# Kernel tuning notes

Hardware: AMD Instinct MI355X
Metric: run time of the kernel (lower is better)

## Reference

```python
import jax, jax.numpy as jnp
import numpy as np

N = 50000          # nodes
E = 1_600_000      # edges (avg degree 32)
D = 128            # input_dim
H = 128            # hidden_dim
EPS = 1e-5


def setup_inputs() -> dict:
    key = jax.random.key(0)
    ks = jax.random.split(key, 8)
    x = jax.random.normal(ks[0], (N, D), jnp.float32)
    edge_index = jax.random.randint(ks[1], (2, E), 0, N)
    message = jax.random.normal(ks[2], (E, H), jnp.float32)

    def lin(k, fin, fout):
        return jax.random.normal(k, (fin, fout), jnp.float32) / np.sqrt(fin).astype(np.float32)

    return {
        "x": x,
        "message": message,
        "W1": lin(ks[3], D + 2 * H, H), "b1": jnp.zeros((H,), jnp.float32),
        "g1": jnp.ones((H,), jnp.float32), "be1": jnp.zeros((H,), jnp.float32),
        "W2": lin(ks[4], H, H), "b2": jnp.zeros((H,), jnp.float32),
        "g2": jnp.ones((H,), jnp.float32), "be2": jnp.zeros((H,), jnp.float32),
        "Wa": lin(ks[5], H, 1), "ba": jnp.zeros((1,), jnp.float32),
        "edge_index": edge_index,
    }


def _batchnorm(h, g, b):
    # training-mode BatchNorm1d: biased batch stats over the node dim
    mu = h.mean(axis=0)
    var = h.var(axis=0)
    return (h - mu) * jax.lax.rsqrt(var + EPS) * g + b


def reference(x, message, W1, b1, g1, be1, W2, b2, g2, be2, Wa, ba, edge_index):
    row, col = edge_index[0], edge_index[1]
    n = x.shape[0]

    def smax(idx):
        m = jax.ops.segment_max(message, idx, num_segments=n)  # [N, H]
        # torch_scatter scatter(reduce='max') leaves empty slots at 0
        return jnp.where(jnp.isfinite(m), m, jnp.zeros_like(m))

    fwd = smax(col)
    bwd = smax(row)
    out = jnp.concatenate([x, fwd, bwd], axis=1)  # [N, D+2H]

    h = jax.nn.relu(_batchnorm(out @ W1 + b1, g1, be1))  # dropout = identity (eval)
    h = jax.nn.relu(_batchnorm(h @ W2 + b2, g2, be2))
    att = jax.nn.sigmoid(h @ Wa + ba).reshape(-1)        # [N]
    return h, att
```

## Files before the change

### kernel.cpp

```cpp
#include <hip/hip_runtime.h>
#include <math.h>

#define N_NODES 50000
#define N_EDGES 1600000
#define DIM 128
#define EPS 1e-5f
#define CAP 96
#define CONVB 2048

typedef short bf16x8 __attribute__((ext_vector_type(8)));
typedef float f32x4 __attribute__((ext_vector_type(4)));
typedef int i32x4 __attribute__((ext_vector_type(4)));
typedef unsigned int u32x2 __attribute__((ext_vector_type(2)));
typedef unsigned short ushort_t;

__device__ __forceinline__ unsigned int f2bf(float f) {
    unsigned int u = __float_as_uint(f);
    return (u + 0x7FFFu + ((u >> 16) & 1u)) >> 16;
}
__device__ __forceinline__ float bf2f(ushort_t u) {
    return __uint_as_float(((unsigned int)u) << 16);
}

__device__ __forceinline__ void wmax(unsigned int w, float& lo, float& hi) {
    lo = fmaxf(lo, __uint_as_float(w << 16));
    hi = fmaxf(hi, __uint_as_float(w & 0xFFFF0000u));
}

__global__ __launch_bounds__(256) void k_prep(const float* __restrict__ W1, const float* __restrict__ W2,
                                              ushort_t* __restrict__ W1t, ushort_t* __restrict__ W2t) {
    int gid = blockIdx.x * 256 + threadIdx.x;
    if (gid < 128 * 384) {
        int j = gid / 384, k = gid % 384;
        W1t[gid] = (ushort_t)f2bf(W1[k * 128 + j]);
    } else {
        int g2 = gid - 128 * 384;
        if (g2 < 128 * 128) {
            int j = g2 / 128, k = g2 % 128;
            W2t[g2] = (ushort_t)f2bf(W2[k * 128 + j]);
        }
    }
}

__global__ __launch_bounds__(256) void k_bucketconv(const int* __restrict__ ei, int* __restrict__ cnt,
                                                    int* __restrict__ slots,
                                                    const f32x4* __restrict__ msg,
                                                    u32x2* __restrict__ msgb) {
    const int b = blockIdx.x;
    if (b & 1) {
        int t = (b >> 1) * 256 + threadIdx.x;
        if (t >= N_EDGES / 4) return;
        int4 r4 = reinterpret_cast<const int4*>(ei)[t];
        int4 c4 = reinterpret_cast<const int4*>(ei + N_EDGES)[t];
        int e = t * 4;
        slots[c4.x * CAP + atomicAdd(&cnt[c4.x], 1)] = e + 0;
        slots[c4.y * CAP + atomicAdd(&cnt[c4.y], 1)] = e + 1;
        slots[c4.z * CAP + atomicAdd(&cnt[c4.z], 1)] = e + 2;
        slots[c4.w * CAP + atomicAdd(&cnt[c4.w], 1)] = e + 3;
        slots[(N_NODES + r4.x) * CAP + atomicAdd(&cnt[N_NODES + r4.x], 1)] = e + 0;
        slots[(N_NODES + r4.y) * CAP + atomicAdd(&cnt[N_NODES + r4.y], 1)] = e + 1;
        slots[(N_NODES + r4.z) * CAP + atomicAdd(&cnt[N_NODES + r4.z], 1)] = e + 2;
        slots[(N_NODES + r4.w) * CAP + atomicAdd(&cnt[N_NODES + r4.w], 1)] = e + 3;
    } else {
        const int cb = b >> 1;
        const size_t total = (size_t)N_EDGES * 32;
        const size_t stride = (size_t)CONVB * 256;
        for (size_t v = (size_t)cb * 256 + threadIdx.x; v < total; v += stride) {
            f32x4 m = __builtin_nontemporal_load(&msg[v]);
            u32x2 o;
            o[0] = f2bf(m[0]) | (f2bf(m[1]) << 16);
            o[1] = f2bf(m[2]) | (f2bf(m[3]) << 16);
            msgb[v] = o;
        }
    }
}

__global__ __launch_bounds__(256) void k_gather(const u32x2* __restrict__ msgb,
                                                const int* __restrict__ slots,
                                                const int* __restrict__ cnt,
                                                ushort_t* __restrict__ fwd,
                                                ushort_t* __restrict__ bwd) {
    const int wid = blockIdx.x * 4 + (threadIdx.x >> 6);
    const int dir = wid & 1;
    const int n = wid >> 1;
    const int lane = threadIdx.x & 63;
    const int q = lane & 31;
    const int h = lane >> 5;
    const int c = cnt[dir * N_NODES + n];
    const int* el = slots + (size_t)(dir * N_NODES + n) * CAP;

    float l0a = -INFINITY, h0a = -INFINITY, l1a = -INFINITY, h1a = -INFINITY;
    float l0b = -INFINITY, h0b = -INFINITY, l1b = -INFINITY, h1b = -INFINITY;
    const int nfull = c >> 2;
    int g = h;
    for (; g + 2 < nfull; g += 4) {
        i32x4 ea = *reinterpret_cast<const i32x4*>(el + g * 4);
        i32x4 eb = *reinterpret_cast<const i32x4*>(el + (g + 2) * 4);
        u32x2 m0 = msgb[(size_t)ea[0] * 32 + q];
        u32x2 m1 = msgb[(size_t)ea[1] * 32 + q];
        u32x2 m2 = msgb[(size_t)ea[2] * 32 + q];
        u32x2 m3 = msgb[(size_t)ea[3] * 32 + q];
        u32x2 m4 = msgb[(size_t)eb[0] * 32 + q];
        u32x2 m5 = msgb[(size_t)eb[1] * 32 + q];
        u32x2 m6 = msgb[(size_t)eb[2] * 32 + q];
        u32x2 m7 = msgb[(size_t)eb[3] * 32 + q];
        wmax(m0[0], l0a, h0a); wmax(m0[1], l1a, h1a);
        wmax(m1[0], l0a, h0a); wmax(m1[1], l1a, h1a);
        wmax(m2[0], l0a, h0a); wmax(m2[1], l1a, h1a);
        wmax(m3[0], l0a, h0a); wmax(m3[1], l1a, h1a);
        wmax(m4[0], l0b, h0b); wmax(m4[1], l1b, h1b);
        wmax(m5[0], l0b, h0b); wmax(m5[1], l1b, h1b);
        wmax(m6[0], l0b, h0b); wmax(m6[1], l1b, h1b);
        wmax(m7[0], l0b, h0b); wmax(m7[1], l1b, h1b);
    }
    for (; g < nfull; g += 2) {
        i32x4 e4 = *reinterpret_cast<const i32x4*>(el + g * 4);
        u32x2 m0 = msgb[(size_t)e4[0] * 32 + q];
        u32x2 m1 = msgb[(size_t)e4[1] * 32 + q];
        u32x2 m2 = msgb[(size_t)e4[2] * 32 + q];
        u32x2 m3 = msgb[(size_t)e4[3] * 32 + q];
        wmax(m0[0], l0a, h0a); wmax(m0[1], l1a, h1a);
        wmax(m1[0], l0a, h0a); wmax(m1[1], l1a, h1a);
        wmax(m2[0], l0a, h0a); wmax(m2[1], l1a, h1a);
        wmax(m3[0], l0a, h0a); wmax(m3[1], l1a, h1a);
    }
    if (h == (nfull & 1)) {
        for (int p = nfull * 4; p < c; ++p) {
            u32x2 m = msgb[(size_t)el[p] * 32 + q];
            wmax(m[0], l0b, h0b); wmax(m[1], l1b, h1b);
        }
    }
    float l0 = fmaxf(l0a, l0b), h0 = fmaxf(h0a, h0b);
    float l1 = fmaxf(l1a, l1b), h1 = fmaxf(h1a, h1b);
    l0 = fmaxf(l0, __shfl_xor(l0, 32));
    h0 = fmaxf(h0, __shfl_xor(h0, 32));
    l1 = fmaxf(l1, __shfl_xor(l1, 32));
    h1 = fmaxf(h1, __shfl_xor(h1, 32));

    if (h == 0) {
        u32x2 o;
        if (c == 0) { o[0] = 0u; o[1] = 0u; }
        else {
            o[0] = (__float_as_uint(l0) >> 16) | (__float_as_uint(h0) & 0xFFFF0000u);
            o[1] = (__float_as_uint(l1) >> 16) | (__float_as_uint(h1) & 0xFFFF0000u);
        }
        *reinterpret_cast<u32x2*>((dir ? bwd : fwd) + n * DIM + q * 4) = o;
    }
}


__global__ __launch_bounds__(256) void k_gemm1(const float* __restrict__ x,
                                               const ushort_t* __restrict__ fwd,
                                               const ushort_t* __restrict__ bwd,
                                               const ushort_t* __restrict__ W1t,
                                               const float* __restrict__ b1,
                                               ushort_t* __restrict__ h1b,
                                               float* __restrict__ stats) {
    __shared__ uint4 rowsA4[512];
    __shared__ uint4 Wt4[1024];
    __shared__ float bias[128];
    __shared__ float s_sum[128], s_sq[128];
    char* rowsA = (char*)rowsA4;
    char* Wt = (char*)Wt4;

    const int tid = threadIdx.x;
    const int wid = tid >> 6;
    const int lane = tid & 63;
    const int ln15 = lane & 15;
    const int kb16 = (lane >> 4) * 16;
    const int n0 = blockIdx.x * 64;
    const int rA = wid * 16 + ln15;
    const int rsw = (rA & 7) << 4;

    if (tid < 128) { bias[tid] = b1[tid]; s_sum[tid] = 0.0f; s_sq[tid] = 0.0f; }

    f32x4 acc[8];
#pragma unroll
    for (int i = 0; i < 8; ++i) acc[i] = (f32x4){0.0f, 0.0f, 0.0f, 0.0f};

    for (int c = 0; c < 6; ++c) {
        const int koff = (c & 1) * 64;
        __syncthreads();
        if (c < 2) {
#pragma unroll
            for (int i = 0; i < 2; ++i) {
                int g = tid + i * 256;
                int r = g >> 3, k8 = g & 7;
                int n = n0 + r;
                f32x4 v0 = {0.f, 0.f, 0.f, 0.f}, v1 = v0;
                if (n < N_NODES) {
                    const f32x4* p = reinterpret_cast<const f32x4*>(x + n * DIM + koff + k8 * 8);
                    v0 = __builtin_nontemporal_load(p);
                    v1 = __builtin_nontemporal_load(p + 1);
                }
                ushort_t pk[8] = {(ushort_t)f2bf(v0[0]), (ushort_t)f2bf(v0[1]),
                                  (ushort_t)f2bf(v0[2]), (ushort_t)f2bf(v0[3]),
                                  (ushort_t)f2bf(v1[0]), (ushort_t)f2bf(v1[1]),
                                  (ushort_t)f2bf(v1[2]), (ushort_t)f2bf(v1[3])};
                *(uint4*)(rowsA + ((r * 128 + k8 * 16) ^ ((r & 7) << 4))) = *(const uint4*)pk;
            }
        } else {
            const ushort_t* src16 = (c < 4) ? fwd : bwd;
#pragma unroll
            for (int i = 0; i < 2; ++i) {
                int g = tid + i * 256;
                int r = g >> 3, k8 = g & 7;
                int n = n0 + r;
                uint4 v = make_uint4(0u, 0u, 0u, 0u);
                if (n < N_NODES) v = *reinterpret_cast<const uint4*>(src16 + n * DIM + koff + k8 * 8);
                *(uint4*)(rowsA + ((r * 128 + k8 * 16) ^ ((r & 7) << 4))) = v;
            }
        }
#pragma unroll
        for (int i = 0; i < 4; ++i) {
            int g = tid + i * 256;
            int j = g >> 3, k8 = g & 7;
            uint4 w = *reinterpret_cast<const uint4*>(W1t + j * 384 + c * 64 + k8 * 8);
            *(uint4*)(Wt + ((j * 128 + k8 * 16) ^ ((j & 7) << 4))) = w;
        }
        __syncthreads();
#pragma unroll
        for (int ks = 0; ks < 2; ++ks) {
            bf16x8 a = *(bf16x8*)(rowsA + ((rA * 128 + ks * 64 + kb16) ^ rsw));
#pragma unroll
            for (int ct = 0; ct < 8; ++ct) {
                int j = ct * 16 + ln15;
                bf16x8 b = *(bf16x8*)(Wt + ((j * 128 + ks * 64 + kb16) ^ ((j & 7) << 4)));
                acc[ct] = __builtin_amdgcn_mfma_f32_16x16x32_bf16(a, b, acc[ct], 0, 0, 0);
            }
        }
    }
    __syncthreads();
    const int jcol = ln15;
#pragma unroll
    for (int ct = 0; ct < 8; ++ct) {
        int j = ct * 16 + jcol;
        float bj = bias[j];
        float s = 0.0f, q = 0.0f;
#pragma unroll
        for (int r = 0; r < 4; ++r) {
            int n = n0 + wid * 16 + (lane >> 4) * 4 + r;
            if (n < N_NODES) {
                float v = acc[ct][r] + bj;
                h1b[n * DIM + j] = (ushort_t)f2bf(v);
                s += v; q += v * v;
            }
        }
        s += __shfl_xor(s, 16); s += __shfl_xor(s, 32);
        q += __shfl_xor(q, 16); q += __shfl_xor(q, 32);
        if ((lane >> 4) == 0) { atomicAdd(&s_sum[j], s); atomicAdd(&s_sq[j], q); }
    }
    __syncthreads();
    if (tid < 128) {
        atomicAdd(&stats[tid], s_sum[tid]);
        atomicAdd(&stats[128 + tid], s_sq[tid]);
    }
}

__global__ __launch_bounds__(256) void k_gemm2(const ushort_t* __restrict__ h1b,
                                               const ushort_t* __restrict__ W2t,
                                               const float* __restrict__ b2,
                                               const float* __restrict__ g1,
                                               const float* __restrict__ be1,
                                               ushort_t* __restrict__ h2b,
                                               float* __restrict__ stats) {
    __shared__ uint4 rowsA4[512];
    __shared__ uint4 Wt4[1024];
    __shared__ float bias[128];
    __shared__ float ssc[128], ssh[128];
    __shared__ float s_sum[128], s_sq[128];
    char* rowsA = (char*)rowsA4;
    char* Wt = (char*)Wt4;

    const int tid = threadIdx.x;
    const int wid = tid >> 6;
    const int lane = tid & 63;
    const int ln15 = lane & 15;
    const int kb16 = (lane >> 4) * 16;
    const int n0 = blockIdx.x * 64;
    const int rA = wid * 16 + ln15;
    const int rsw = (rA & 7) << 4;

    if (tid < 128) {
        float mu = stats[tid] * (1.0f / N_NODES);
        float var = stats[128 + tid] * (1.0f / N_NODES) - mu * mu;
        float sc = rsqrtf(var + EPS) * g1[tid];
        ssc[tid] = sc;
        ssh[tid] = be1[tid] - mu * sc;
        bias[tid] = b2[tid];
        s_sum[tid] = 0.0f; s_sq[tid] = 0.0f;
    }

    f32x4 acc[8];
#pragma unroll
    for (int i = 0; i < 8; ++i) acc[i] = (f32x4){0.0f, 0.0f, 0.0f, 0.0f};

    for (int c = 0; c < 2; ++c) {
        const int koff = c * 64;
        __syncthreads();
#pragma unroll
        for (int i = 0; i < 2; ++i) {
            int g = tid + i * 256;
            int r = g >> 3, k8 = g & 7;
            int n = n0 + r;
            ushort_t pk[8] = {0, 0, 0, 0, 0, 0, 0, 0};
            if (n < N_NODES) {
                uint4 raw = *reinterpret_cast<const uint4*>(h1b + n * DIM + koff + k8 * 8);
                const ushort_t* rp = (const ushort_t*)&raw;
#pragma unroll
                for (int t = 0; t < 8; ++t) {
                    int kk = koff + k8 * 8 + t;
                    float v = fmaxf(bf2f(rp[t]) * ssc[kk] + ssh[kk], 0.0f);
                    pk[t] = (ushort_t)f2bf(v);
                }
            }
            *(uint4*)(rowsA + ((r * 128 + k8 * 16) ^ ((r & 7) << 4))) = *(const uint4*)pk;
        }
#pragma unroll
        for (int i = 0; i < 4; ++i) {
            int g = tid + i * 256;
            int j = g >> 3, k8 = g & 7;
            uint4 w = *reinterpret_cast<const uint4*>(W2t + j * 128 + c * 64 + k8 * 8);
            *(uint4*)(Wt + ((j * 128 + k8 * 16) ^ ((j & 7) << 4))) = w;
        }
        __syncthreads();
#pragma unroll
        for (int ks = 0; ks < 2; ++ks) {
            bf16x8 a = *(bf16x8*)(rowsA + ((rA * 128 + ks * 64 + kb16) ^ rsw));
#pragma unroll
            for (int ct = 0; ct < 8; ++ct) {
                int j = ct * 16 + ln15;
                bf16x8 b = *(bf16x8*)(Wt + ((j * 128 + ks * 64 + kb16) ^ ((j & 7) << 4)));
                acc[ct] = __builtin_amdgcn_mfma_f32_16x16x32_bf16(a, b, acc[ct], 0, 0, 0);
            }
        }
    }
    __syncthreads();
    const int jcol = ln15;
#pragma unroll
    for (int ct = 0; ct < 8; ++ct) {
        int j = ct * 16 + jcol;
        float bj = bias[j];
        float s = 0.0f, q = 0.0f;
#pragma unroll
        for (int r = 0; r < 4; ++r) {
            int n = n0 + wid * 16 + (lane >> 4) * 4 + r;
            if (n < N_NODES) {
                float v = acc[ct][r] + bj;
                h2b[n * DIM + j] = (ushort_t)f2bf(v);
                s += v; q += v * v;
            }
        }
        s += __shfl_xor(s, 16); s += __shfl_xor(s, 32);
        q += __shfl_xor(q, 16); q += __shfl_xor(q, 32);
        if ((lane >> 4) == 0) { atomicAdd(&s_sum[j], s); atomicAdd(&s_sq[j], q); }
    }
    __syncthreads();
    if (tid < 128) {
        atomicAdd(&stats[256 + tid], s_sum[tid]);
        atomicAdd(&stats[384 + tid], s_sq[tid]);
    }
}

__global__ __launch_bounds__(256) void k_final(const ushort_t* __restrict__ h2b,
                                               const float* __restrict__ stats,
                                               const float* __restrict__ g2,
                                               const float* __restrict__ be2,
                                               const float* __restrict__ Wa,
                                               const float* __restrict__ ba,
                                               float* __restrict__ out) {
    const int lane = threadIdx.x & 63;
    const int wv = threadIdx.x >> 6;
    const int n = blockIdx.x * 4 + wv;
    if (n >= N_NODES) return;
    const int j0 = lane, j1 = lane + 64;

    float mu0 = stats[256 + j0] * (1.0f / N_NODES);
    float var0 = stats[384 + j0] * (1.0f / N_NODES) - mu0 * mu0;
    float sc0 = rsqrtf(var0 + EPS) * g2[j0];
    float sh0 = be2[j0] - mu0 * sc0;
    float mu1 = stats[256 + j1] * (1.0f / N_NODES);
    float var1 = stats[384 + j1] * (1.0f / N_NODES) - mu1 * mu1;
    float sc1 = rsqrtf(var1 + EPS) * g2[j1];
    float sh1 = be2[j1] - mu1 * sc1;

    float v0 = fmaxf(bf2f(h2b[n * DIM + j0]) * sc0 + sh0, 0.0f);
    float v1 = fmaxf(bf2f(h2b[n * DIM + j1]) * sc1 + sh1, 0.0f);
    out[n * DIM + j0] = v0;
    out[n * DIM + j1] = v1;

    float p = v0 * Wa[j0] + v1 * Wa[j1];
#pragma unroll
    for (int off = 32; off > 0; off >>= 1) p += __shfl_down(p, off);
    if (lane == 0) out[N_NODES * DIM + n] = 1.0f / (1.0f + expf(-(p + ba[0])));
}

extern "C" void kernel_launch(void* const* d_in, const int* in_sizes, int n_in,
                              void* d_out, int out_size, void* d_ws, size_t ws_size,
                              hipStream_t stream) {
    const float* x   = (const float*)d_in[0];
    const float* msg = (const float*)d_in[1];
    const float* W1  = (const float*)d_in[2];
    const float* b1  = (const float*)d_in[3];
    const float* g1  = (const float*)d_in[4];
    const float* be1 = (const float*)d_in[5];
    const float* W2  = (const float*)d_in[6];
    const float* b2  = (const float*)d_in[7];
    const float* g2  = (const float*)d_in[8];
    const float* be2 = (const float*)d_in[9];
    const float* Wa  = (const float*)d_in[10];
    const float* ba  = (const float*)d_in[11];
    const int*   ei  = (const int*)d_in[12];

    float*    stats = (float*)d_ws;
    ushort_t* fwdb  = (ushort_t*)(stats + 512);
    ushort_t* bwdb  = fwdb + N_NODES * DIM;
    int*      cnt   = (int*)(bwdb + N_NODES * DIM);
    int*      slots = cnt + 2 * N_NODES;
    ushort_t* W1t   = (ushort_t*)(slots + 2 * N_NODES * CAP);
    ushort_t* W2t   = W1t + 128 * 384;
    u32x2*    msgb  = (u32x2*)(W2t + 128 * 128 + 128);

    ushort_t* h1b = (ushort_t*)d_out;
    ushort_t* h2b = fwdb;
    float*    out = (float*)d_out;

    (void)hipMemsetAsync(stats, 0, 512 * sizeof(float), stream);
    (void)hipMemsetAsync(cnt, 0, 2 * N_NODES * sizeof(int), stream);
    k_prep<<<(128 * 384 + 128 * 128 + 255) / 256, 256, 0, stream>>>(W1, W2, W1t, W2t);
    k_bucketconv<<<2 * CONVB, 256, 0, stream>>>(ei, cnt, slots, (const f32x4*)msg, msgb);
    k_gather<<<(2 * N_NODES) / 4, 256, 0, stream>>>(msgb, slots, cnt, fwdb, bwdb);
    k_gemm1<<<(N_NODES + 63) / 64, 256, 0, stream>>>(x, fwdb, bwdb, W1t, b1, h1b, stats);
    k_gemm2<<<(N_NODES + 63) / 64, 256, 0, stream>>>(h1b, W2t, b2, g1, be1, h2b, stats);
    k_final<<<(N_NODES + 3) / 4, 256, 0, stream>>>(h2b, stats, g2, be2, Wa, ba, out);
}
```

Before: 576.1 us.

## Fuse message bf16 conversion into forward segment-max gather over col buckets

Column bucketing moves into its own kernel that runs first. The forward segment-max is then fused with the fp32-to-bf16 message conversion: each message row is read once in fp32 through col buckets, maxed in full precision and written out as bf16. Row bucketing runs in the same launch, and the backward gather reads the bf16 copy afterwards. This removes one full pass over the message tensor, but the fp32 reads become random row gathers instead of a streaming pass, and it adds an extra launch.

```diff
diff --git a/kernel.cpp b/kernel.cpp
--- a/kernel.cpp
+++ b/kernel.cpp
@@ -6,7 +6,7 @@
 #define DIM 128
 #define EPS 1e-5f
 #define CAP 96
-#define CONVB 2048
+#define BINB 1563
 
 typedef short bf16x8 __attribute__((ext_vector_type(8)));
 typedef float f32x4 __attribute__((ext_vector_type(4)));
@@ -21,7 +21,12 @@
 __device__ __forceinline__ float bf2f(ushort_t u) {
     return __uint_as_float(((unsigned int)u) << 16);
 }
-
+__device__ __forceinline__ f32x4 v4max(f32x4 a, f32x4 b) {
+    f32x4 r;
+    r[0] = fmaxf(a[0], b[0]); r[1] = fmaxf(a[1], b[1]);
+    r[2] = fmaxf(a[2], b[2]); r[3] = fmaxf(a[3], b[3]);
+    return r;
+}
 __device__ __forceinline__ void wmax(unsigned int w, float& lo, float& hi) {
     lo = fmaxf(lo, __uint_as_float(w << 16));
     hi = fmaxf(hi, __uint_as_float(w & 0xFFFF0000u));
@@ -42,52 +47,113 @@
     }
 }
 
-__global__ __launch_bounds__(256) void k_bucketconv(const int* __restrict__ ei, int* __restrict__ cnt,
-                                                    int* __restrict__ slots,
-                                                    const f32x4* __restrict__ msg,
-                                                    u32x2* __restrict__ msgb) {
+__global__ __launch_bounds__(256) void k_bucket_col(const int* __restrict__ ei, int* __restrict__ cnt,
+                                                    int* __restrict__ slots) {
+    int t = blockIdx.x * 256 + threadIdx.x;
+    if (t >= N_EDGES / 4) return;
+    int4 c4 = reinterpret_cast<const int4*>(ei + N_EDGES)[t];
+    int e = t * 4;
+    slots[c4.x * CAP + atomicAdd(&cnt[c4.x], 1)] = e + 0;
+    slots[c4.y * CAP + atomicAdd(&cnt[c4.y], 1)] = e + 1;
+    slots[c4.z * CAP + atomicAdd(&cnt[c4.z], 1)] = e + 2;
+    slots[c4.w * CAP + atomicAdd(&cnt[c4.w], 1)] = e + 3;
+}
+
+__global__ __launch_bounds__(256) void k_fwdconv_rowbin(const f32x4* __restrict__ msg,
+                                                        const int* __restrict__ ei,
+                                                        int* __restrict__ cnt,
+                                                        int* __restrict__ slots,
+                                                        u32x2* __restrict__ msgb,
+                                                        ushort_t* __restrict__ fwdb) {
     const int b = blockIdx.x;
     if (b & 1) {
         int t = (b >> 1) * 256 + threadIdx.x;
         if (t >= N_EDGES / 4) return;
         int4 r4 = reinterpret_cast<const int4*>(ei)[t];
-        int4 c4 = reinterpret_cast<const int4*>(ei + N_EDGES)[t];
         int e = t * 4;
-        slots[c4.x * CAP + atomicAdd(&cnt[c4.x], 1)] = e + 0;
-        slots[c4.y * CAP + atomicAdd(&cnt[c4.y], 1)] = e + 1;
-        slots[c4.z * CAP + atomicAdd(&cnt[c4.z], 1)] = e + 2;
-        slots[c4.w * CAP + atomicAdd(&cnt[c4.w], 1)] = e + 3;
         slots[(N_NODES + r4.x) * CAP + atomicAdd(&cnt[N_NODES + r4.x], 1)] = e + 0;
         slots[(N_NODES + r4.y) * CAP + atomicAdd(&cnt[N_NODES + r4.y], 1)] = e + 1;
         slots[(N_NODES + r4.z) * CAP + atomicAdd(&cnt[N_NODES + r4.z], 1)] = e + 2;
         slots[(N_NODES + r4.w) * CAP + atomicAdd(&cnt[N_NODES + r4.w], 1)] = e + 3;
-    } else {
-        const int cb = b >> 1;
-        const size_t total = (size_t)N_EDGES * 32;
-        const size_t stride = (size_t)CONVB * 256;
-        for (size_t v = (size_t)cb * 256 + threadIdx.x; v < total; v += stride) {
-            f32x4 m = __builtin_nontemporal_load(&msg[v]);
-            u32x2 o;
-            o[0] = f2bf(m[0]) | (f2bf(m[1]) << 16);
-            o[1] = f2bf(m[2]) | (f2bf(m[3]) << 16);
-            msgb[v] = o;
-        }
-    }
-}
-
-__global__ __launch_bounds__(256) void k_gather(const u32x2* __restrict__ msgb,
-                                                const int* __restrict__ slots,
-                                                const int* __restrict__ cnt,
-                                                ushort_t* __restrict__ fwd,
-                                                ushort_t* __restrict__ bwd) {
-    const int wid = blockIdx.x * 4 + (threadIdx.x >> 6);
-    const int dir = wid & 1;
-    const int n = wid >> 1;
+        return;
+    }
+    const int n = (b >> 1) * 4 + (threadIdx.x >> 6);
     const int lane = threadIdx.x & 63;
     const int q = lane & 31;
     const int h = lane >> 5;
-    const int c = cnt[dir * N_NODES + n];
-    const int* el = slots + (size_t)(dir * N_NODES + n) * CAP;
+    const int c = cnt[n];
+    const int* el = slots + (size_t)n * CAP;
+
+    f32x4 acc0 = {-INFINITY, -INFINITY, -INFINITY, -INFINITY};
+    f32x4 acc1 = acc0;
+    const int nfull = c >> 2;
+    int g = h;
+    for (; g + 2 < nfull; g += 4) {
+        i32x4 ea = *reinterpret_cast<const i32x4*>(el + g * 4);
+        i32x4 eb = *reinterpret_cast<const i32x4*>(el + (g + 2) * 4);
+#pragma unroll
+        for (int i = 0; i < 4; ++i) {
+            size_t off = (size_t)ea[i] * 32 + q;
+            f32x4 m = __builtin_nontemporal_load(&msg[off]);
+            u32x2 o; o[0] = f2bf(m[0]) | (f2bf(m[1]) << 16); o[1] = f2bf(m[2]) | (f2bf(m[3]) << 16);
+            msgb[off] = o;
+            acc0 = v4max(acc0, m);
+        }
+#pragma unroll
+        for (int i = 0; i < 4; ++i) {
+            size_t off = (size_t)eb[i] * 32 + q;
+            f32x4 m = __builtin_nontemporal_load(&msg[off]);
+            u32x2 o; o[0] = f2bf(m[0]) | (f2bf(m[1]) << 16); o[1] = f2bf(m[2]) | (f2bf(m[3]) << 16);
+            msgb[off] = o;
+            acc1 = v4max(acc1, m);
+        }
+    }
+    for (; g < nfull; g += 2) {
+        i32x4 e4 = *reinterpret_cast<const i32x4*>(el + g * 4);
+#pragma unroll
+        for (int i = 0; i < 4; ++i) {
+            size_t off = (size_t)e4[i] * 32 + q;
+            f32x4 m = __builtin_nontemporal_load(&msg[off]);
+            u32x2 o; o[0] = f2bf(m[0]) | (f2bf(m[1]) << 16); o[1] = f2bf(m[2]) | (f2bf(m[3]) << 16);
+            msgb[off] = o;
+            acc0 = v4max(acc0, m);
+        }
+    }
+    if (h == (nfull & 1)) {
+        for (int p = nfull * 4; p < c; ++p) {
+            size_t off = (size_t)el[p] * 32 + q;
+            f32x4 m = __builtin_nontemporal_load(&msg[off]);
+            u32x2 o; o[0] = f2bf(m[0]) | (f2bf(m[1]) << 16); o[1] = f2bf(m[2]) | (f2bf(m[3]) << 16);
+            msgb[off] = o;
+            acc1 = v4max(acc1, m);
+        }
+    }
+    f32x4 acc = v4max(acc0, acc1);
+    acc[0] = fmaxf(acc[0], __shfl_xor(acc[0], 32));
+    acc[1] = fmaxf(acc[1], __shfl_xor(acc[1], 32));
+    acc[2] = fmaxf(acc[2], __shfl_xor(acc[2], 32));
+    acc[3] = fmaxf(acc[3], __shfl_xor(acc[3], 32));
+    if (h == 0) {
+        u32x2 o;
+        if (c == 0) { o[0] = 0u; o[1] = 0u; }
+        else {
+            o[0] = f2bf(acc[0]) | (f2bf(acc[1]) << 16);
+            o[1] = f2bf(acc[2]) | (f2bf(acc[3]) << 16);
+        }
+        *reinterpret_cast<u32x2*>(fwdb + n * DIM + q * 4) = o;
+    }
+}
+
+__global__ __launch_bounds__(256) void k_gather_bwd(const u32x2* __restrict__ msgb,
+                                                    const int* __restrict__ slots,
+                                                    const int* __restrict__ cnt,
+                                                    ushort_t* __restrict__ bwdb) {
+    const int n = blockIdx.x * 4 + (threadIdx.x >> 6);
+    const int lane = threadIdx.x & 63;
+    const int q = lane & 31;
+    const int h = lane >> 5;
+    const int c = cnt[N_NODES + n];
+    const int* el = slots + (size_t)(N_NODES + n) * CAP;
 
     float l0a = -INFINITY, h0a = -INFINITY, l1a = -INFINITY, h1a = -INFINITY;
     float l0b = -INFINITY, h0b = -INFINITY, l1b = -INFINITY, h1b = -INFINITY;
@@ -136,7 +202,6 @@
     h0 = fmaxf(h0, __shfl_xor(h0, 32));
     l1 = fmaxf(l1, __shfl_xor(l1, 32));
     h1 = fmaxf(h1, __shfl_xor(h1, 32));
-
     if (h == 0) {
         u32x2 o;
         if (c == 0) { o[0] = 0u; o[1] = 0u; }
@@ -144,7 +209,7 @@
             o[0] = (__float_as_uint(l0) >> 16) | (__float_as_uint(h0) & 0xFFFF0000u);
             o[1] = (__float_as_uint(l1) >> 16) | (__float_as_uint(h1) & 0xFFFF0000u);
         }
-        *reinterpret_cast<u32x2*>((dir ? bwd : fwd) + n * DIM + q * 4) = o;
+        *reinterpret_cast<u32x2*>(bwdb + n * DIM + q * 4) = o;
     }
 }
 
@@ -428,8 +493,9 @@
     (void)hipMemsetAsync(stats, 0, 512 * sizeof(float), stream);
     (void)hipMemsetAsync(cnt, 0, 2 * N_NODES * sizeof(int), stream);
     k_prep<<<(128 * 384 + 128 * 128 + 255) / 256, 256, 0, stream>>>(W1, W2, W1t, W2t);
-    k_bucketconv<<<2 * CONVB, 256, 0, stream>>>(ei, cnt, slots, (const f32x4*)msg, msgb);
-    k_gather<<<(2 * N_NODES) / 4, 256, 0, stream>>>(msgb, slots, cnt, fwdb, bwdb);
+    k_bucket_col<<<BINB, 256, 0, stream>>>(ei, cnt, slots);
+    k_fwdconv_rowbin<<<2 * (N_NODES / 4), 256, 0, stream>>>((const f32x4*)msg, ei, cnt, slots, msgb, fwdb);
+    k_gather_bwd<<<N_NODES / 4, 256, 0, stream>>>(msgb, slots, cnt, bwdb);
     k_gemm1<<<(N_NODES + 63) / 64, 256, 0, stream>>>(x, fwdb, bwdb, W1t, b1, h1b, stats);
     k_gemm2<<<(N_NODES + 63) / 64, 256, 0, stream>>>(h1b, W2t, b2, g1, be1, h2b, stats);
     k_final<<<(N_NODES + 3) / 4, 256, 0, stream>>>(h2b, stats, g2, be2, Wa, ba, out);
```

After: 610.1 us. 5.9% more time.
